# Kernel tuning notes

Measured on AMD Instinct MI355X. Metric: run time of the kernel, lower is better.

Reference implementation:

```python
import jax, jax.numpy as jnp
import numpy as np

# ---- statevector quantum-circuit simulation helpers ----

def _rx(theta):
    # RX gate; theta scalar -> [2,2], theta [T] -> [T,2,2]
    c = jnp.cos(theta / 2.0).astype(jnp.complex64)
    s = (-1j * jnp.sin(theta / 2.0)).astype(jnp.complex64)
    return jnp.stack([jnp.stack([c, s], -1), jnp.stack([s, c], -1)], -2)


def _rot(phi, theta, omega):
    # PennyLane Rot = RZ(omega) RY(theta) RZ(phi)
    c = jnp.cos(theta / 2.0).astype(jnp.complex64)
    s = jnp.sin(theta / 2.0).astype(jnp.complex64)
    ep = jnp.exp(-0.5j * (omega + phi)).astype(jnp.complex64)
    em = jnp.exp(0.5j * (omega - phi)).astype(jnp.complex64)
    return jnp.stack([jnp.stack([ep * c, -jnp.conj(em) * s], -1),
                      jnp.stack([em * s, jnp.conj(ep) * c], -1)], -2)


def _apply1(state, gate, wire):
    # state: [T] + [2]*n ; gate: [2,2] (shared) or [T,2,2] (per-token encoding)
    state = jnp.moveaxis(state, 1 + wire, -1)
    if gate.ndim == 3:
        state = jnp.einsum('t...a,tba->t...b', state, gate)
    else:
        state = jnp.einsum('...a,ba->...b', state, gate)
    return jnp.moveaxis(state, -1, 1 + wire)


def _cnot(state, c, t):
    st = jnp.moveaxis(state, (1 + c, 1 + t), (-2, -1))
    st = jnp.stack([st[..., 0, :], st[..., 1, ::-1]], axis=-2)
    return jnp.moveaxis(st, (-2, -1), (1 + c, 1 + t))


def _zexp(state, wire):
    p = state.real ** 2 + state.imag ** 2
    p = jnp.moveaxis(p, 1 + wire, -1).reshape(p.shape[0], -1, 2)
    return jnp.sum(p[..., 0] - p[..., 1], axis=1)


def _qcircuit(x, w, scalar_out):
    # x: [T, n] angle-encoded inputs; w: [3n] (+1 if scalar_out) trainable angles
    T, n = x.shape
    state = jnp.zeros((T,) + (2,) * n, jnp.complex64)
    state = state.at[(slice(None),) + (0,) * n].set(1.0)
    for i in range(n):                       # angle encoding
        state = _apply1(state, _rx(x[:, i]), i)
    if n > 1:                                # ring entanglement
        for i in range(n):
            state = _cnot(state, i, (i + 1) % n)
    for i in range(n):                       # trainable rotations
        state = _apply1(state, _rot(w[3 * i], w[3 * i + 1], w[3 * i + 2]), i)
    if scalar_out:                           # query/key: extra RX, measure Z on wire 0
        state = _apply1(state, _rx(w[3 * n]), 0)
        return _zexp(state, 0)
    return jnp.stack([_zexp(state, i) for i in range(n)], axis=-1)


def _layernorm(x, eps=1e-5):
    m = jnp.mean(x, -1, keepdims=True)
    v = jnp.mean((x - m) ** 2, -1, keepdims=True)
    return (x - m) / jnp.sqrt(v + eps)


def setup_inputs() -> dict:
    key = jax.random.key(0)
    k = jax.random.split(key, 5)
    B, S, E, H = 16, 512, 8, 2
    d = E // H
    return {
        'x': jax.random.normal(k[0], (B, S, E), jnp.float32),
        'Vw': jax.random.normal(k[1], (H, 3 * d), jnp.float32),
        'Qw': jax.random.normal(k[2], (H, 3 * d + 1), jnp.float32),
        'Kw': jax.random.normal(k[3], (H, 3 * d + 1), jnp.float32),
        'Mw': jax.random.normal(k[4], (3 * E,), jnp.float32),
    }


def reference(x, Vw, Qw, Kw, Mw):
    B, S, E = x.shape
    H = Vw.shape[0]
    d = E // H
    scale = 1.0 / np.sqrt(d).astype(np.float32)
    xn = _layernorm(x)
    outs = []
    for h in range(H):  # fixed small loop over structurally distinct heads
        xh = xn[..., h * d:(h + 1) * d].reshape(B * S, d)
        V = _qcircuit(xh, Vw[h], False).reshape(B, S, d)
        Q = _qcircuit(xh, Qw[h], True).reshape(B, S)
        K = _qcircuit(xh, Kw[h], True).reshape(B, S)
        A = -(Q[:, :, None] - K[:, None, :]) ** 2          # [B,S,S]
        P = jax.nn.softmax(A * scale, axis=-1)
        outs.append(jnp.einsum('bij,bjd->bid', P, V))
    head_out = jnp.concatenate(outs, axis=-1)              # [B,S,E]
    merged = _qcircuit(head_out.reshape(B * S, E), Mw, False).reshape(B, S, E)
    return merged + x
```

## Files before the change

kernel.cpp:

```cpp
#include <hip/hip_runtime.h>

#define NS 512


__global__ __launch_bounds__(256)
void k_fused(const float* __restrict__ x, const float* __restrict__ Vw,
             const float* __restrict__ Qw, const float* __restrict__ Kw,
             const float* __restrict__ Mw, float* __restrict__ out)
{
    __shared__ float  Qs[2][NS];
    __shared__ float  Ks[2][NS];
    __shared__ float4 Vs[2][NS];
    __shared__ float  HOs[16][8];

    int tid = threadIdx.x;
    int b   = blockIdx.x >> 5;
    int rg  = blockIdx.x & 31;

    float aQ[2], aK[2], vc0[2], vc1[2], vc2[2], vc3[2], vs3[2];
    #pragma unroll
    for (int h = 0; h < 2; ++h) {
        const float* qw = Qw + h*13;
        const float* kw = Kw + h*13;
        const float* vw = Vw + h*12;
        float sT, cT, sB, cB;
        __sincosf(qw[1], &sT, &cT); __sincosf(qw[12], &sB, &cB);
        aQ[h] = cB*cT + sB*sT*__sinf(qw[2]);
        __sincosf(kw[1], &sT, &cT); __sincosf(kw[12], &sB, &cB);
        aK[h] = cB*cT + sB*sT*__sinf(kw[2]);
        vc0[h] = __cosf(vw[1]);
        vc1[h] = __cosf(vw[4]);
        vc2[h] = __cosf(vw[7]);
        float s3; __sincosf(vw[10], &s3, &vc3[h]);
        vs3[h] = s3 * __sinf(vw[9]);
    }

    #pragma unroll
    for (int k = 0; k < 2; ++k) {
        int tl = tid + k*256;
        const float4* xp = (const float4*)(x + (b*NS + tl)*8);
        float4 xa = xp[0], xb = xp[1];
        float xv[8] = {xa.x, xa.y, xa.z, xa.w, xb.x, xb.y, xb.z, xb.w};
        float m = 0.f;
        #pragma unroll
        for (int e = 0; e < 8; ++e) m += xv[e];
        m *= 0.125f;
        float var = 0.f;
        #pragma unroll
        for (int e = 0; e < 8; ++e) { float d = xv[e]-m; var += d*d; }
        float inv = rsqrtf(var*0.125f + 1e-5f);

        #pragma unroll
        for (int h = 0; h < 2; ++h) {
            float cg[4], sg[4];
            #pragma unroll
            for (int i = 0; i < 4; ++i)
                __sincosf((xv[h*4+i]-m)*inv, &sg[i], &cg[i]);
            float c01  = cg[0]*cg[1];
            float c123 = cg[1]*cg[2]*cg[3];
            Qs[h][tl] = aQ[h] * c123;
            Ks[h][tl] = aK[h] * c123;
            float4 v;
            v.x = vc0[h] * c123;
            v.y = vc1[h] * c01;
            v.z = vc2[h] * c01 * cg[2];
            v.w = vc3[h] * c01 * cg[2] * cg[3] + vs3[h] * sg[0]*sg[1]*sg[3]*cg[2];
            Vs[h][tl] = v;
        }
    }
    __syncthreads();

    {
        int lane = tid & 63;
        int w    = tid >> 6;
        int task = w*8 + (lane >> 3);
        int l8   = lane & 7;
        int hh   = task >> 4;
        int r    = task & 15;
        int row  = rg*16 + r;
        float q  = Qs[hh][row];

        float sum = 0.f, a0 = 0.f, a1 = 0.f, a2 = 0.f, a3 = 0.f;
        #pragma unroll 8
        for (int k = 0; k < 64; ++k) {
            int j = k*8 + l8;
            float d = q - Ks[hh][j];
            float p = __expf(-0.5f*d*d);
            float4 vv = Vs[hh][j];
            sum += p; a0 += p*vv.x; a1 += p*vv.y; a2 += p*vv.z; a3 += p*vv.w;
        }
        #pragma unroll
        for (int off = 1; off < 8; off <<= 1) {
            sum += __shfl_xor(sum, off, 8);
            a0  += __shfl_xor(a0,  off, 8);
            a1  += __shfl_xor(a1,  off, 8);
            a2  += __shfl_xor(a2,  off, 8);
            a3  += __shfl_xor(a3,  off, 8);
        }
        if (l8 == 0) {
            float rr = 1.0f / sum;
            HOs[r][hh*4 + 0] = a0*rr;
            HOs[r][hh*4 + 1] = a1*rr;
            HOs[r][hh*4 + 2] = a2*rr;
            HOs[r][hh*4 + 3] = a3*rr;
        }
    }
    __syncthreads();

    if (tid < 16) {
        float cT0 = __cosf(Mw[1]);
        float cT1 = __cosf(Mw[4]);
        float cT2 = __cosf(Mw[7]);
        float cT3 = __cosf(Mw[10]);
        float cT4 = __cosf(Mw[13]);
        float cT5 = __cosf(Mw[16]);
        float cT6 = __cosf(Mw[19]);
        float s7w, cT7; __sincosf(Mw[22], &s7w, &cT7);
        float vs77 = s7w * __sinf(Mw[21]);

        int t = b*NS + rg*16 + tid;
        float a[8];
        #pragma unroll
        for (int e = 0; e < 8; ++e) a[e] = HOs[tid][e];

        float ca[8], sa0, sa1, sa7;
        __sincosf(a[0], &sa0, &ca[0]);
        __sincosf(a[1], &sa1, &ca[1]);
        ca[2] = __cosf(a[2]);
        ca[3] = __cosf(a[3]);
        ca[4] = __cosf(a[4]);
        ca[5] = __cosf(a[5]);
        ca[6] = __cosf(a[6]);
        __sincosf(a[7], &sa7, &ca[7]);

        float P1 = ca[0]*ca[1];
        float P2 = P1*ca[2];
        float P3 = P2*ca[3];
        float P4 = P3*ca[4];
        float P5 = P4*ca[5];
        float P6 = P5*ca[6];
        float P7 = P6*ca[7];
        float c34 = ca[3]*ca[4], c56 = ca[5]*ca[6];
        float Q17 = ca[1]*ca[2]*c34*c56*ca[7];
        float M26 = ca[2]*c34*c56;

        const float4* xp = (const float4*)(x + t*8);
        float4 x0 = xp[0], x1 = xp[1];
        float4 o0 = {cT0*Q17 + x0.x, cT1*P1 + x0.y, cT2*P2 + x0.z, cT3*P3 + x0.w};
        float4 o1 = {cT4*P4 + x1.x, cT5*P5 + x1.y, cT6*P6 + x1.z,
                     cT7*P7 + vs77*sa0*sa1*sa7*M26 + x1.w};
        float4* op = (float4*)(out + t*8);
        op[0] = o0; op[1] = o1;
    }
}

extern "C" void kernel_launch(void* const* d_in, const int* in_sizes, int n_in,
                              void* d_out, int out_size, void* d_ws, size_t ws_size,
                              hipStream_t stream) {
    (void)in_sizes; (void)n_in; (void)out_size; (void)d_ws; (void)ws_size;
    const float* x  = (const float*)d_in[0];
    const float* Vw = (const float*)d_in[1];
    const float* Qw = (const float*)d_in[2];
    const float* Kw = (const float*)d_in[3];
    const float* Mw = (const float*)d_in[4];
    float* out = (float*)d_out;

    hipLaunchKernelGGL(k_fused, dim3(512), dim3(256), 0, stream,
                       x, Vw, Qw, Kw, Mw, out);
}
```

Before: 11.35 us.

## Share K/V float4 loads across two query rows and factor head scales out

Q, K and V are no longer stored separately. One float4 per token holds the shared cosine products, and the per-head scalar factors (aQ, aK, vc0..2) are applied at use time, which shrinks shared memory and the number of writes. Each 16-lane group now handles two query rows at once, so every shared-memory K/V load is reused for two exponentials. The cost is more accumulator registers and a longer 16-lane shuffle reduction.

```diff
diff --git a/kernel.cpp b/kernel.cpp
--- a/kernel.cpp
+++ b/kernel.cpp
@@ -8,32 +8,28 @@
              const float* __restrict__ Qw, const float* __restrict__ Kw,
              const float* __restrict__ Mw, float* __restrict__ out)
 {
-    __shared__ float  Qs[2][NS];
-    __shared__ float  Ks[2][NS];
-    __shared__ float4 Vs[2][NS];
+    __shared__ float4 As4[2][NS];
     __shared__ float  HOs[16][8];
 
     int tid = threadIdx.x;
     int b   = blockIdx.x >> 5;
     int rg  = blockIdx.x & 31;
 
-    float aQ[2], aK[2], vc0[2], vc1[2], vc2[2], vc3[2], vs3[2];
-    #pragma unroll
-    for (int h = 0; h < 2; ++h) {
-        const float* qw = Qw + h*13;
-        const float* kw = Kw + h*13;
-        const float* vw = Vw + h*12;
-        float sT, cT, sB, cB;
-        __sincosf(qw[1], &sT, &cT); __sincosf(qw[12], &sB, &cB);
-        aQ[h] = cB*cT + sB*sT*__sinf(qw[2]);
-        __sincosf(kw[1], &sT, &cT); __sincosf(kw[12], &sB, &cB);
-        aK[h] = cB*cT + sB*sT*__sinf(kw[2]);
-        vc0[h] = __cosf(vw[1]);
-        vc1[h] = __cosf(vw[4]);
-        vc2[h] = __cosf(vw[7]);
-        float s3; __sincosf(vw[10], &s3, &vc3[h]);
-        vs3[h] = s3 * __sinf(vw[9]);
-    }
+    float sT, cT, sB, cB, s3;
+    __sincosf(Qw[1],  &sT, &cT); __sincosf(Qw[12], &sB, &cB);
+    float aQ0 = cB*cT + sB*sT*__sinf(Qw[2]);
+    __sincosf(Qw[14], &sT, &cT); __sincosf(Qw[25], &sB, &cB);
+    float aQ1 = cB*cT + sB*sT*__sinf(Qw[15]);
+    __sincosf(Kw[1],  &sT, &cT); __sincosf(Kw[12], &sB, &cB);
+    float aK0 = cB*cT + sB*sT*__sinf(Kw[2]);
+    __sincosf(Kw[14], &sT, &cT); __sincosf(Kw[25], &sB, &cB);
+    float aK1 = cB*cT + sB*sT*__sinf(Kw[15]);
+    float vc0_0 = __cosf(Vw[1]),  vc1_0 = __cosf(Vw[4]),  vc2_0 = __cosf(Vw[7]);
+    float vc3_0; __sincosf(Vw[10], &s3, &vc3_0);
+    float vs3_0 = s3 * __sinf(Vw[9]);
+    float vc0_1 = __cosf(Vw[13]), vc1_1 = __cosf(Vw[16]), vc2_1 = __cosf(Vw[19]);
+    float vc3_1; __sincosf(Vw[22], &s3, &vc3_1);
+    float vs3_1 = s3 * __sinf(Vw[21]);
 
     #pragma unroll
     for (int k = 0; k < 2; ++k) {
@@ -50,22 +46,24 @@
         for (int e = 0; e < 8; ++e) { float d = xv[e]-m; var += d*d; }
         float inv = rsqrtf(var*0.125f + 1e-5f);
 
+        float cg[8], sg[8];
         #pragma unroll
-        for (int h = 0; h < 2; ++h) {
-            float cg[4], sg[4];
-            #pragma unroll
-            for (int i = 0; i < 4; ++i)
-                __sincosf((xv[h*4+i]-m)*inv, &sg[i], &cg[i]);
-            float c01  = cg[0]*cg[1];
-            float c123 = cg[1]*cg[2]*cg[3];
-            Qs[h][tl] = aQ[h] * c123;
-            Ks[h][tl] = aK[h] * c123;
-            float4 v;
-            v.x = vc0[h] * c123;
-            v.y = vc1[h] * c01;
-            v.z = vc2[h] * c01 * cg[2];
-            v.w = vc3[h] * c01 * cg[2] * cg[3] + vs3[h] * sg[0]*sg[1]*sg[3]*cg[2];
-            Vs[h][tl] = v;
+        for (int i = 0; i < 8; ++i)
+            __sincosf((xv[i]-m)*inv, &sg[i], &cg[i]);
+
+        {
+            float A = cg[1]*cg[2]*cg[3];
+            float B = cg[0]*cg[1];
+            float C = B*cg[2];
+            float W = vc3_0*(C*cg[3]) + vs3_0*(sg[0]*sg[1]*sg[3]*cg[2]);
+            As4[0][tl] = make_float4(A, B, C, W);
+        }
+        {
+            float A = cg[5]*cg[6]*cg[7];
+            float B = cg[4]*cg[5];
+            float C = B*cg[6];
+            float W = vc3_1*(C*cg[7]) + vs3_1*(sg[4]*sg[5]*sg[7]*cg[6]);
+            As4[1][tl] = make_float4(A, B, C, W);
         }
     }
     __syncthreads();
@@ -73,36 +71,55 @@
     {
         int lane = tid & 63;
         int w    = tid >> 6;
-        int task = w*8 + (lane >> 3);
-        int l8   = lane & 7;
-        int hh   = task >> 4;
-        int r    = task & 15;
-        int row  = rg*16 + r;
-        float q  = Qs[hh][row];
+        int t16  = w*4 + (lane >> 4);
+        int l16  = lane & 15;
+        int hh   = t16 >> 3;
+        int rp   = t16 & 7;
+        int ra   = rg*16 + rp*2;
 
-        float sum = 0.f, a0 = 0.f, a1 = 0.f, a2 = 0.f, a3 = 0.f;
+        float aK = hh ? aK1 : aK0;
+        float aQ = hh ? aQ1 : aQ0;
+        const float* Af = (const float*)As4;
+        float qa = aQ * Af[(hh*NS + ra)*4];
+        float qb = aQ * Af[(hh*NS + ra + 1)*4];
+
+        float s0=0.f, A0=0.f, B0=0.f, C0=0.f, W0=0.f;
+        float s1=0.f, A1=0.f, B1=0.f, C1=0.f, W1=0.f;
         #pragma unroll 8
-        for (int k = 0; k < 64; ++k) {
-            int j = k*8 + l8;
-            float d = q - Ks[hh][j];
-            float p = __expf(-0.5f*d*d);
-            float4 vv = Vs[hh][j];
-            sum += p; a0 += p*vv.x; a1 += p*vv.y; a2 += p*vv.z; a3 += p*vv.w;
+        for (int k = 0; k < 32; ++k) {
+            int j = k*16 + l16;
+            float4 P = As4[hh][j];
+            float kv = aK * P.x;
+            float da = qa - kv, db = qb - kv;
+            float pa = __expf(-0.5f*da*da);
+            float pb = __expf(-0.5f*db*db);
+            s0 += pa; A0 += pa*P.x; B0 += pa*P.y; C0 += pa*P.z; W0 += pa*P.w;
+            s1 += pb; A1 += pb*P.x; B1 += pb*P.y; C1 += pb*P.z; W1 += pb*P.w;
         }
         #pragma unroll
-        for (int off = 1; off < 8; off <<= 1) {
-            sum += __shfl_xor(sum, off, 8);
-            a0  += __shfl_xor(a0,  off, 8);
-            a1  += __shfl_xor(a1,  off, 8);
-            a2  += __shfl_xor(a2,  off, 8);
-            a3  += __shfl_xor(a3,  off, 8);
+        for (int off = 1; off < 16; off <<= 1) {
+            s0 += __shfl_xor(s0, off, 16); A0 += __shfl_xor(A0, off, 16);
+            B0 += __shfl_xor(B0, off, 16); C0 += __shfl_xor(C0, off, 16);
+            W0 += __shfl_xor(W0, off, 16);
+            s1 += __shfl_xor(s1, off, 16); A1 += __shfl_xor(A1, off, 16);
+            B1 += __shfl_xor(B1, off, 16); C1 += __shfl_xor(C1, off, 16);
+            W1 += __shfl_xor(W1, off, 16);
         }
-        if (l8 == 0) {
-            float rr = 1.0f / sum;
-            HOs[r][hh*4 + 0] = a0*rr;
-            HOs[r][hh*4 + 1] = a1*rr;
-            HOs[r][hh*4 + 2] = a2*rr;
-            HOs[r][hh*4 + 3] = a3*rr;
+        if (l16 < 2) {
+            float ss = l16 ? s1 : s0;
+            float sA = l16 ? A1 : A0;
+            float sBv= l16 ? B1 : B0;
+            float sC = l16 ? C1 : C0;
+            float sW = l16 ? W1 : W0;
+            float r  = 1.0f / ss;
+            float v0 = hh ? vc0_1 : vc0_0;
+            float v1 = hh ? vc1_1 : vc1_0;
+            float v2 = hh ? vc2_1 : vc2_0;
+            int rr = rp*2 + l16;
+            HOs[rr][hh*4 + 0] = v0*sA*r;
+            HOs[rr][hh*4 + 1] = v1*sBv*r;
+            HOs[rr][hh*4 + 2] = v2*sC*r;
+            HOs[rr][hh*4 + 3] = sW*r;
         }
     }
     __syncthreads();
```

New measurement: 11.60 us. 1.02x slower.
